# Performance work log

Measured on AMD Instinct MI355X. Metric: run time of the kernel, lower is better.

Reference implementation:

```python
import jax, jax.numpy as jnp
import numpy as np

N, E, F_IN, H, C = 10000, 320000, 256, 256, 40


def setup_inputs() -> dict:
    key = jax.random.key(0)
    ks = jax.random.split(key, 12)
    inp = {
        "x": jax.random.normal(ks[0], (N, F_IN), dtype=jnp.float32),
        "edge_index": jax.random.randint(ks[1], (2, E), 0, N, dtype=jnp.int64),
    }
    dims = [(F_IN, H), (H, H), (H, H), (H, H), (H, C)]
    for i, (din, dout) in enumerate(dims, start=1):
        scale = 1.0 / np.sqrt(din)
        inp[f"W{i}"] = jax.random.normal(ks[1 + i], (din, dout), dtype=jnp.float32) * scale
        inp[f"b{i}"] = jnp.zeros((dout,), dtype=jnp.float32)
    return inp


def _gcn_norm(edge_index, num_nodes, dtype):
    # GCNConv: add self-loops, symmetric normalization D^-1/2 (A+I) D^-1/2
    loops = jnp.arange(num_nodes, dtype=edge_index.dtype)
    src = jnp.concatenate([edge_index[0], loops])
    dst = jnp.concatenate([edge_index[1], loops])
    deg = jax.ops.segment_sum(jnp.ones_like(dst, dtype=dtype), dst, num_segments=num_nodes)
    dinv = jnp.where(deg > 0, deg ** -0.5, 0.0).astype(dtype)
    norm = dinv[src] * dinv[dst]  # [E+N]
    return src, dst, norm


def _conv(h, src, dst, norm, W, b, num_nodes):
    # linear transform then gather-scale-scatter aggregation
    h = h @ W                           # [N, dout]
    msg = h[src] * norm[:, None]        # [E+N, dout]
    return jax.ops.segment_sum(msg, dst, num_segments=num_nodes) + b


def reference(x, edge_index, W1, b1, W2, b2, W3, b3, W4, b4, W5, b5):
    num_nodes = x.shape[0]
    src, dst, norm = _gcn_norm(edge_index, num_nodes, x.dtype)
    h = jax.nn.relu(_conv(x, src, dst, norm, W1, b1, num_nodes))
    h = jax.nn.relu(_conv(h, src, dst, norm, W2, b2, num_nodes))
    h = jax.nn.relu(_conv(h, src, dst, norm, W3, b3, num_nodes))
    h = jax.nn.relu(_conv(h, src, dst, norm, W4, b4, num_nodes))
    logits = _conv(h, src, dst, norm, W5, b5, num_nodes)
    return jax.nn.log_softmax(logits, axis=1), logits
```

## Files before the change

kernel.cpp:

```cpp
#include <hip/hip_runtime.h>
#include <hip/hip_bf16.h>

#define N_NODES 10000
#define N_EDGES 320000
#define HDIM    256
#define NCLS    40
#define WTOT    273448

typedef __attribute__((ext_vector_type(8))) short short8;
typedef __attribute__((ext_vector_type(4))) float floatx4;
typedef unsigned long long ull;
typedef unsigned short ushort;

__device__ __forceinline__ float bf2f(ushort u) {
    union { unsigned int i; float f; } v; v.i = ((unsigned int)u) << 16; return v.f;
}
__device__ __forceinline__ ushort f2bf(float f) {
    __hip_bfloat16 h = __float2bfloat16(f);
    return *reinterpret_cast<ushort*>(&h);
}

__device__ __forceinline__ void detect_flags(const void* x, const void* ei,
                                             int* sflags) {
    const int tid = threadIdx.x;
    if (tid < 64) {
        const ushort* u = (const ushort*)x;
        int e = (u[2 * tid] >> 7) & 0xFF;
        ull badmask = __ballot(e < 100 || e > 140);
        const int* ii = (const int*)ei;
        ull oddnz = __ballot(ii[2 * tid + 1] != 0);
        if (tid == 0) {
            sflags[0] = (__popcll(badmask) >= 8) ? 1 : 0;
            sflags[1] = (oddnz == 0) ? 1 : 0;
        }
    }
    __syncthreads();
}


struct PrepArgs {
    const void* x;
    const void* ei;
    const void* wsrc[10];
    ushort* wdst[10];
    int woffs[11];
    ushort* xb;
    int* src32;
    int* dst32;
    int* cnt;
    ushort* tbuf;
    ushort* hbuf;
    int* flags;
};

#define PREP_XB 2500
#define PREP_WB 1069
#define PREP_EB 1250
#define PREP_TOTAL (PREP_XB + PREP_WB + PREP_EB + 1)

__global__ __launch_bounds__(256)
void prep_kernel(PrepArgs a) {
    __shared__ int sflags[2];
    detect_flags(a.x, a.ei, sflags);
    const int f32 = sflags[0];
    const int b = blockIdx.x;

    if (b < PREP_XB) {
        int i4 = b * 256 + threadIdx.x;
        if (f32) {
            float4 v = ((const float4*)a.x)[i4];
            ull p = (ull)f2bf(v.x) | ((ull)f2bf(v.y) << 16) |
                    ((ull)f2bf(v.z) << 32) | ((ull)f2bf(v.w) << 48);
            ((ull*)a.xb)[i4] = p;
        } else {
            ((ull*)a.xb)[i4] = ((const ull*)a.x)[i4];
        }
    } else if (b < PREP_XB + PREP_WB) {
        int i = (b - PREP_XB) * 256 + threadIdx.x;
        if (i < WTOT) {
            int t = 0;
#pragma unroll
            for (int k = 1; k < 10; ++k) t += (i >= a.woffs[k]);
            int local = i - a.woffs[t];
            ushort v;
            if (f32) v = f2bf(((const float*)a.wsrc[t])[local]);
            else     v = ((const ushort*)a.wsrc[t])[local];
            a.wdst[t][local] = v;
        }
    } else if (b < PREP_XB + PREP_WB + PREP_EB) {
        int e = (b - PREP_XB - PREP_WB) * 256 + threadIdx.x;
        const int* ii = (const int*)a.ei;
        int s, d;
        if (sflags[1]) { s = ii[2 * e]; d = ii[2 * (N_EDGES + e)]; }
        else           { s = ii[e];     d = ii[N_EDGES + e]; }
        s = ((unsigned)s < N_NODES) ? s : 0;
        d = ((unsigned)d < N_NODES) ? d : 0;
        a.src32[e] = s;
        a.dst32[e] = d;
        atomicAdd(&a.cnt[d], 1);
    } else {
        int t = threadIdx.x;
        if (t < 64)       ((ull*)(a.tbuf + (size_t)N_NODES * 256))[t] = 0;
        else if (t < 128) ((ull*)(a.hbuf + (size_t)N_NODES * 256))[t - 64] = 0;
        if (t == 0) { a.flags[0] = sflags[0]; a.flags[1] = sflags[1]; }
    }
}


__global__ __launch_bounds__(1024)
void scan_dinv_kernel(const int* __restrict__ cnt, int* __restrict__ offs,
                      int* __restrict__ woff, float* __restrict__ dinv) {
    __shared__ int wsum[16];
    const int t = threadIdx.x;
    const int lane = t & 63;
    const int wv = t >> 6;
    const int base = t * 10;

    int c[10];
    int s = 0;
#pragma unroll
    for (int j = 0; j < 10; ++j) {
        int i = base + j;
        c[j] = (i < N_NODES) ? cnt[i] : 0;
        s += c[j];
    }

    int inc = s;
#pragma unroll
    for (int o = 1; o < 64; o <<= 1) {
        int v = __shfl_up(inc, o);
        if (lane >= o) inc += v;
    }
    if (lane == 63) wsum[wv] = inc;
    __syncthreads();

    if (wv == 0 && lane < 16) {
        int w = wsum[lane];
        int wi = w;
#pragma unroll
        for (int o = 1; o < 16; o <<= 1) {
            int v = __shfl_up(wi, o);
            if (lane >= o) wi += v;
        }
        wsum[lane] = wi - w;
    }
    __syncthreads();

    int run = wsum[wv] + (inc - s);
#pragma unroll
    for (int j = 0; j < 10; ++j) {
        int i = base + j;
        if (i < N_NODES) {
            offs[i] = run;
            woff[i] = run;
            dinv[i] = rsqrtf((float)c[j] + 1.0f);
            run += c[j];
        }
    }
}


#define FILL_BLKS 1250
#define GEMM1_YT  78
#define FG_TOTAL  (FILL_BLKS + 8 * GEMM1_YT)

__global__ __launch_bounds__(256)
void fillgemm_kernel(const int* __restrict__ src, const int* __restrict__ dst,
                     int* __restrict__ woff, int* __restrict__ csr,
                     const ushort* __restrict__ A, const ushort* __restrict__ W,
                     const float* __restrict__ dinv, ushort* __restrict__ T) {
    const int b = blockIdx.x;
    if (b < FILL_BLKS) {
        int e = b * 256 + threadIdx.x;
        int d = dst[e];
        int p = atomicAdd(&woff[d], 1);
        csr[p] = src[e];
        return;
    }
    const int g = b - FILL_BLKS;
    const int lane = threadIdx.x & 63;
    const int wave = threadIdx.x >> 6;
    const int m = lane & 15;
    const int quad = lane >> 4;
    const int c0 = (g & 7) * 32;
    const int by = g >> 3;

    short8 bfrag[2][8];
#pragma unroll
    for (int t = 0; t < 2; ++t)
#pragma unroll
        for (int s = 0; s < 8; ++s)
#pragma unroll
            for (int j = 0; j < 8; ++j)
                bfrag[t][s][j] = (short)W[(size_t)(s * 32 + quad * 8 + j) * 256 + c0 + t * 16 + m];

    const int step = GEMM1_YT * 4;
    for (int rt = by * 4 + wave; rt < N_NODES / 16; rt += step) {
        const int r0 = rt * 16;
        floatx4 acc0 = {0.f, 0.f, 0.f, 0.f};
        floatx4 acc1 = {0.f, 0.f, 0.f, 0.f};
        const ushort* arow = A + (size_t)(r0 + m) * 256 + quad * 8;
#pragma unroll
        for (int s = 0; s < 8; ++s) {
            short8 af = *(const short8*)(arow + s * 32);
            acc0 = __builtin_amdgcn_mfma_f32_16x16x32_bf16(af, bfrag[0][s], acc0, 0, 0, 0);
            acc1 = __builtin_amdgcn_mfma_f32_16x16x32_bf16(af, bfrag[1][s], acc1, 0, 0, 0);
        }
#pragma unroll
        for (int r = 0; r < 4; ++r) {
            int row = r0 + quad * 4 + r;
            float di = dinv[row];
            T[(size_t)row * 256 + c0 + m]      = f2bf(acc0[r] * di);
            T[(size_t)row * 256 + c0 + 16 + m] = f2bf(acc1[r] * di);
        }
    }
}


__global__ __launch_bounds__(256)
void gemm256_kernel(const ushort* __restrict__ A, const ushort* __restrict__ W,
                    const float* __restrict__ dinv, ushort* __restrict__ T) {
    const int lane = threadIdx.x & 63;
    const int wave = threadIdx.x >> 6;
    const int m = lane & 15;
    const int quad = lane >> 4;
    const int c0 = blockIdx.x * 32;

    short8 bfrag[2][8];
#pragma unroll
    for (int t = 0; t < 2; ++t)
#pragma unroll
        for (int s = 0; s < 8; ++s)
#pragma unroll
            for (int j = 0; j < 8; ++j)
                bfrag[t][s][j] = (short)W[(size_t)(s * 32 + quad * 8 + j) * 256 + c0 + t * 16 + m];

    const int step = gridDim.y * 4;
    for (int rt = blockIdx.y * 4 + wave; rt < N_NODES / 16; rt += step) {
        const int r0 = rt * 16;
        floatx4 acc0 = {0.f, 0.f, 0.f, 0.f};
        floatx4 acc1 = {0.f, 0.f, 0.f, 0.f};
        const ushort* arow = A + (size_t)(r0 + m) * 256 + quad * 8;
#pragma unroll
        for (int s = 0; s < 8; ++s) {
            short8 af = *(const short8*)(arow + s * 32);
            acc0 = __builtin_amdgcn_mfma_f32_16x16x32_bf16(af, bfrag[0][s], acc0, 0, 0, 0);
            acc1 = __builtin_amdgcn_mfma_f32_16x16x32_bf16(af, bfrag[1][s], acc1, 0, 0, 0);
        }
#pragma unroll
        for (int r = 0; r < 4; ++r) {
            int row = r0 + quad * 4 + r;
            float di = dinv[row];
            T[(size_t)row * 256 + c0 + m]      = f2bf(acc0[r] * di);
            T[(size_t)row * 256 + c0 + 16 + m] = f2bf(acc1[r] * di);
        }
    }
}


__global__ __launch_bounds__(256)
void gemm40_kernel(const ushort* __restrict__ A, const ushort* __restrict__ W,
                   const float* __restrict__ dinv, float* __restrict__ T) {
    const int lane = threadIdx.x & 63;
    const int wave = threadIdx.x >> 6;
    const int m = lane & 15;
    const int quad = lane >> 4;
    const int col = blockIdx.x * 16 + m;
    const bool colok = col < NCLS;

    short8 bfrag[8];
#pragma unroll
    for (int s = 0; s < 8; ++s)
#pragma unroll
        for (int j = 0; j < 8; ++j)
            bfrag[s][j] = colok ? (short)W[(size_t)(s * 32 + quad * 8 + j) * NCLS + col] : (short)0;

    const int step = gridDim.y * 4;
    for (int rt = blockIdx.y * 4 + wave; rt < N_NODES / 16; rt += step) {
        const int r0 = rt * 16;
        floatx4 acc = {0.f, 0.f, 0.f, 0.f};
        const ushort* arow = A + (size_t)(r0 + m) * 256 + quad * 8;
#pragma unroll
        for (int s = 0; s < 8; ++s) {
            short8 af = *(const short8*)(arow + s * 32);
            acc = __builtin_amdgcn_mfma_f32_16x16x32_bf16(af, bfrag[s], acc, 0, 0, 0);
        }
        if (colok) {
#pragma unroll
            for (int r = 0; r < 4; ++r) {
                int row = r0 + quad * 4 + r;
                T[(size_t)row * NCLS + col] = acc[r] * dinv[row];
            }
        }
    }
}


__device__ __forceinline__ void accum16(float* acc, int4 r) {
    int d[4] = {r.x, r.y, r.z, r.w};
#pragma unroll
    for (int k = 0; k < 4; ++k) {
        union { int i; float f; } lo, hi;
        lo.i = d[k] << 16;
        hi.i = d[k] & 0xffff0000;
        acc[2 * k]     += lo.f;
        acc[2 * k + 1] += hi.f;
    }
}

__global__ __launch_bounds__(256)
void agg256_kernel(const ushort* __restrict__ T,
                   const int* __restrict__ csr, const int* __restrict__ offs,
                   const int* __restrict__ cnt, const float* __restrict__ dinv,
                   const ushort* __restrict__ bias,
                   ushort* __restrict__ H) {
    const int node = blockIdx.x * 4 + (threadIdx.x >> 6);
    const int lane = threadIdx.x & 63;
    const int half = lane >> 5;
    const int q = lane & 31;
    const int start = offs[node];
    const int count = cnt[node];
    const float di = dinv[node];

    float acc[8];
    {
        int sinit = half ? N_NODES : node;
        int4 r = *(const int4*)(T + (size_t)sinit * 256 + q * 8);
#pragma unroll
        for (int k = 0; k < 4; ++k) {
            union { int i; float f; } lo, hi;
            int d = (&r.x)[k];
            lo.i = d << 16; hi.i = d & 0xffff0000;
            acc[2 * k] = lo.f; acc[2 * k + 1] = hi.f;
        }
    }

    for (int bj = 0; bj < count; bj += 64) {
        int mrem = count - bj;
        int mm = mrem < 64 ? mrem : 64;
        int idxv = (lane < mm) ? csr[start + bj + lane] : N_NODES;
        int j2 = 0;
        for (; j2 + 8 <= mm; j2 += 8) {
            int s0 = __shfl(idxv, j2 + half);
            int s1 = __shfl(idxv, j2 + 2 + half);
            int s2 = __shfl(idxv, j2 + 4 + half);
            int s3 = __shfl(idxv, j2 + 6 + half);
            int4 r0 = *(const int4*)(T + (size_t)s0 * 256 + q * 8);
            int4 r1 = *(const int4*)(T + (size_t)s1 * 256 + q * 8);
            int4 r2 = *(const int4*)(T + (size_t)s2 * 256 + q * 8);
            int4 r3 = *(const int4*)(T + (size_t)s3 * 256 + q * 8);
            accum16(acc, r0); accum16(acc, r1); accum16(acc, r2); accum16(acc, r3);
        }
        for (; j2 < mm; j2 += 2) {
            int s = __shfl(idxv, j2 + half);
            int4 r = *(const int4*)(T + (size_t)s * 256 + q * 8);
            accum16(acc, r);
        }
    }

#pragma unroll
    for (int i = 0; i < 8; ++i) acc[i] += __shfl_xor(acc[i], 32);

    if (half == 0) {
        int4 bv = *(const int4*)(bias + q * 8);
        int out_d[4];
#pragma unroll
        for (int k = 0; k < 4; ++k) {
            union { int i; float f; } lo, hi;
            int d = (&bv.x)[k];
            lo.i = d << 16; hi.i = d & 0xffff0000;
            float v0 = fmaxf(acc[2 * k] * di + lo.f, 0.f);
            float v1 = fmaxf(acc[2 * k + 1] * di + hi.f, 0.f);
            out_d[k] = (int)f2bf(v0) | ((int)f2bf(v1) << 16);
        }
        *(int4*)(H + (size_t)node * 256 + q * 8) = *(int4*)out_d;
    }
}


__global__ __launch_bounds__(256)
void aggsoft_kernel(const float* __restrict__ T,
                    const int* __restrict__ csr, const int* __restrict__ offs,
                    const int* __restrict__ cnt, const float* __restrict__ dinv,
                    const ushort* __restrict__ bias,
                    void* __restrict__ out, const int* __restrict__ flags) {
    const int node = blockIdx.x * 4 + (threadIdx.x >> 6);
    const int lane = threadIdx.x & 63;
    const int start = offs[node];
    const int count = cnt[node];
    const float di = dinv[node];

    float acc = (lane < NCLS) ? T[(size_t)node * NCLS + lane] : 0.f;
    for (int bj = 0; bj < count; bj += 64) {
        int mrem = count - bj;
        int mm = mrem < 64 ? mrem : 64;
        int idxv = (lane < mm) ? csr[start + bj + lane] : 0;
        int jj = 0;
        for (; jj + 4 <= mm; jj += 4) {
            int s0 = __shfl(idxv, jj + 0);
            int s1 = __shfl(idxv, jj + 1);
            int s2 = __shfl(idxv, jj + 2);
            int s3 = __shfl(idxv, jj + 3);
            if (lane < NCLS) {
                float t0 = T[(size_t)s0 * NCLS + lane];
                float t1 = T[(size_t)s1 * NCLS + lane];
                float t2 = T[(size_t)s2 * NCLS + lane];
                float t3 = T[(size_t)s3 * NCLS + lane];
                acc += t0 + t1 + t2 + t3;
            }
        }
        for (; jj < mm; ++jj) {
            int s = __shfl(idxv, jj);
            if (lane < NCLS) acc += T[(size_t)s * NCLS + lane];
        }
    }

    float l = (lane < NCLS) ? (acc * di + bf2f(bias[lane])) : -INFINITY;
    float mx = l;
#pragma unroll
    for (int o = 32; o > 0; o >>= 1) mx = fmaxf(mx, __shfl_xor(mx, o));
    float e = (lane < NCLS) ? __expf(l - mx) : 0.f;
    float sum = e;
#pragma unroll
    for (int o = 32; o > 0; o >>= 1) sum += __shfl_xor(sum, o);
    float ls = l - mx - __logf(sum);
    if (lane < NCLS) {
        size_t i0 = (size_t)node * NCLS + lane;
        size_t i1 = (size_t)N_NODES * NCLS + i0;
        if (flags[0]) {
            ((float*)out)[i0] = ls;
            ((float*)out)[i1] = l;
        } else {
            ((ushort*)out)[i0] = f2bf(ls);
            ((ushort*)out)[i1] = f2bf(l);
        }
    }
}


static inline size_t alup(size_t x) { return (x + 255) & ~(size_t)255; }

extern "C" void kernel_launch(void* const* d_in, const int* in_sizes, int n_in,
                              void* d_out, int out_size, void* d_ws, size_t ws_size,
                              hipStream_t stream) {
    char* w = (char*)d_ws;
    int* flags   = (int*)w;           w += alup(16);
    float* dinv  = (float*)w;         w += alup(N_NODES * 4);
    int* cnt     = (int*)w;           w += alup(N_NODES * 4);
    int* offs    = (int*)w;           w += alup(N_NODES * 4);
    int* woff    = (int*)w;           w += alup(N_NODES * 4);
    int* src32   = (int*)w;           w += alup(N_EDGES * 4);
    int* dst32   = (int*)w;           w += alup(N_EDGES * 4);
    int* csr     = (int*)w;           w += alup(N_EDGES * 4);
    ushort* xb   = (ushort*)w;        w += alup((size_t)N_NODES * HDIM * 2);
    ushort* wb[5]; ushort* bb[5];
    for (int l = 0; l < 5; ++l) {
        int wn = (l < 4) ? HDIM * HDIM : HDIM * NCLS;
        int bn = (l < 4) ? HDIM : NCLS;
        wb[l] = (ushort*)w; w += alup((size_t)wn * 2);
        bb[l] = (ushort*)w; w += alup((size_t)bn * 2);
    }
    ushort* tbuf = (ushort*)w;        w += alup((size_t)(N_NODES + 16) * HDIM * 2);
    ushort* hbuf = (ushort*)w;        w += alup((size_t)(N_NODES + 16) * HDIM * 2);
    float* t5    = (float*)w;         w += alup((size_t)N_NODES * NCLS * 4);

    hipMemsetAsync(cnt, 0, N_NODES * 4, stream);

    PrepArgs pa;
    pa.x = d_in[0];
    pa.ei = d_in[1];
    int sizes[10] = { HDIM * HDIM, HDIM, HDIM * HDIM, HDIM, HDIM * HDIM, HDIM,
                      HDIM * HDIM, HDIM, HDIM * NCLS, NCLS };
    int run = 0;
    for (int t = 0; t < 10; ++t) {
        pa.wsrc[t] = d_in[2 + t];
        pa.wdst[t] = (t & 1) ? bb[t >> 1] : wb[t >> 1];
        pa.woffs[t] = run;
        run += sizes[t];
    }
    pa.woffs[10] = run;
    pa.xb = xb; pa.src32 = src32; pa.dst32 = dst32; pa.cnt = cnt;
    pa.tbuf = tbuf; pa.hbuf = hbuf; pa.flags = flags;

    prep_kernel<<<PREP_TOTAL, 256, 0, stream>>>(pa);
    scan_dinv_kernel<<<1, 1024, 0, stream>>>(cnt, offs, woff, dinv);
    fillgemm_kernel<<<FG_TOTAL, 256, 0, stream>>>(src32, dst32, woff, csr,
                                                  xb, wb[0], dinv, tbuf);

    const int aggblk = N_NODES / 4;

    agg256_kernel<<<aggblk, 256, 0, stream>>>(tbuf, csr, offs, cnt, dinv, bb[0], hbuf);
    for (int l = 1; l < 4; ++l) {
        gemm256_kernel<<<dim3(8, 78), 256, 0, stream>>>(hbuf, wb[l], dinv, tbuf);
        agg256_kernel<<<aggblk, 256, 0, stream>>>(tbuf, csr, offs, cnt, dinv, bb[l], hbuf);
    }
    gemm40_kernel<<<dim3(3, 80), 256, 0, stream>>>(hbuf, wb[4], dinv, t5);
    aggsoft_kernel<<<2500, 256, 0, stream>>>(t5, csr, offs, cnt, dinv, bb[4], d_out, flags);
}
```

Measured before the change: 264.9 us.

## Split aggregation feature dim across two blocks, vectorize weight prep

The 256-feature aggregation kernel now launches twice as many blocks, each handling half of the feature columns for a node. Each wave splits into four 16-lane groups that gather different neighbors at once, which doubles the number of independent gathers in flight per wave, and a two-step shuffle reduction combines them. Output uses nontemporal stores, and launch bounds request higher occupancy. Weight conversion in the prep kernel now processes four elements per thread with vector loads. The cost is that neighbor index lists and degrees are read twice, one extra shuffle reduction is added, and each gather row segment is only 256 bytes.

```diff
diff --git a/kernel.cpp b/kernel.cpp
--- a/kernel.cpp
+++ b/kernel.cpp
@@ -6,9 +6,11 @@
 #define HDIM    256
 #define NCLS    40
 #define WTOT    273448
+#define WQUADS  68362
 
 typedef __attribute__((ext_vector_type(8))) short short8;
 typedef __attribute__((ext_vector_type(4))) float floatx4;
+typedef __attribute__((ext_vector_type(4))) int intx4;
 typedef unsigned long long ull;
 typedef unsigned short ushort;
 
@@ -54,7 +56,7 @@
 };
 
 #define PREP_XB 2500
-#define PREP_WB 1069
+#define PREP_WB 268
 #define PREP_EB 1250
 #define PREP_TOTAL (PREP_XB + PREP_WB + PREP_EB + 1)
 
@@ -77,15 +79,21 @@
         }
     } else if (b < PREP_XB + PREP_WB) {
         int i = (b - PREP_XB) * 256 + threadIdx.x;
-        if (i < WTOT) {
+        if (i < WQUADS) {
+            int i4 = i * 4;
             int t = 0;
 #pragma unroll
-            for (int k = 1; k < 10; ++k) t += (i >= a.woffs[k]);
-            int local = i - a.woffs[t];
-            ushort v;
-            if (f32) v = f2bf(((const float*)a.wsrc[t])[local]);
-            else     v = ((const ushort*)a.wsrc[t])[local];
-            a.wdst[t][local] = v;
+            for (int k = 1; k < 10; ++k) t += (i4 >= a.woffs[k]);
+            int local = i4 - a.woffs[t];
+            ull p;
+            if (f32) {
+                float4 v = *(const float4*)((const float*)a.wsrc[t] + local);
+                p = (ull)f2bf(v.x) | ((ull)f2bf(v.y) << 16) |
+                    ((ull)f2bf(v.z) << 32) | ((ull)f2bf(v.w) << 48);
+            } else {
+                p = *(const ull*)((const ushort*)a.wsrc[t] + local);
+            }
+            *(ull*)(a.wdst[t] + local) = p;
         }
     } else if (b < PREP_XB + PREP_WB + PREP_EB) {
         int e = (b - PREP_XB - PREP_WB) * 256 + threadIdx.x;
@@ -296,7 +304,7 @@
 }
 
 
-__device__ __forceinline__ void accum16(float* acc, int4 r) {
+__device__ __forceinline__ void accum16(float* acc, intx4 r) {
     int d[4] = {r.x, r.y, r.z, r.w};
 #pragma unroll
     for (int k = 0; k < 4; ++k) {
@@ -308,28 +316,36 @@
     }
 }
 
-__global__ __launch_bounds__(256)
+#define AGG_BLKS 5000
+
+__global__ __launch_bounds__(256, 4)
 void agg256_kernel(const ushort* __restrict__ T,
                    const int* __restrict__ csr, const int* __restrict__ offs,
                    const int* __restrict__ cnt, const float* __restrict__ dinv,
                    const ushort* __restrict__ bias,
                    ushort* __restrict__ H) {
-    const int node = blockIdx.x * 4 + (threadIdx.x >> 6);
+    const int bid = blockIdx.x;
+    const int h = (bid >= 2500) ? 1 : 0;
+    const int local = h ? (bid - 2500) : bid;
+    const int wave = threadIdx.x >> 6;
+    const int node = local * 4 + wave;
     const int lane = threadIdx.x & 63;
-    const int half = lane >> 5;
-    const int q = lane & 31;
+    const int quarter = lane >> 4;
+    const int q = lane & 15;
+    const int cbase = h * 128 + q * 8;
+
     const int start = offs[node];
     const int count = cnt[node];
     const float di = dinv[node];
 
     float acc[8];
     {
-        int sinit = half ? N_NODES : node;
-        int4 r = *(const int4*)(T + (size_t)sinit * 256 + q * 8);
+        int sinit = quarter ? N_NODES : node;
+        intx4 r = *(const intx4*)(T + (size_t)sinit * 256 + cbase);
 #pragma unroll
         for (int k = 0; k < 4; ++k) {
             union { int i; float f; } lo, hi;
-            int d = (&r.x)[k];
+            int d = r[k];
             lo.i = d << 16; hi.i = d & 0xffff0000;
             acc[2 * k] = lo.f; acc[2 * k + 1] = hi.f;
         }
@@ -340,40 +356,43 @@
         int mm = mrem < 64 ? mrem : 64;
         int idxv = (lane < mm) ? csr[start + bj + lane] : N_NODES;
         int j2 = 0;
-        for (; j2 + 8 <= mm; j2 += 8) {
-            int s0 = __shfl(idxv, j2 + half);
-            int s1 = __shfl(idxv, j2 + 2 + half);
-            int s2 = __shfl(idxv, j2 + 4 + half);
-            int s3 = __shfl(idxv, j2 + 6 + half);
-            int4 r0 = *(const int4*)(T + (size_t)s0 * 256 + q * 8);
-            int4 r1 = *(const int4*)(T + (size_t)s1 * 256 + q * 8);
-            int4 r2 = *(const int4*)(T + (size_t)s2 * 256 + q * 8);
-            int4 r3 = *(const int4*)(T + (size_t)s3 * 256 + q * 8);
+        for (; j2 + 16 <= mm; j2 += 16) {
+            int s0 = __shfl(idxv, j2 + 0  + quarter);
+            int s1 = __shfl(idxv, j2 + 4  + quarter);
+            int s2 = __shfl(idxv, j2 + 8  + quarter);
+            int s3 = __shfl(idxv, j2 + 12 + quarter);
+            intx4 r0 = *(const intx4*)(T + (size_t)s0 * 256 + cbase);
+            intx4 r1 = *(const intx4*)(T + (size_t)s1 * 256 + cbase);
+            intx4 r2 = *(const intx4*)(T + (size_t)s2 * 256 + cbase);
+            intx4 r3 = *(const intx4*)(T + (size_t)s3 * 256 + cbase);
             accum16(acc, r0); accum16(acc, r1); accum16(acc, r2); accum16(acc, r3);
         }
-        for (; j2 < mm; j2 += 2) {
-            int s = __shfl(idxv, j2 + half);
-            int4 r = *(const int4*)(T + (size_t)s * 256 + q * 8);
+        for (; j2 < mm; j2 += 4) {
+            int s = __shfl(idxv, j2 + quarter);
+            intx4 r = *(const intx4*)(T + (size_t)s * 256 + cbase);
             accum16(acc, r);
         }
     }
 
 #pragma unroll
-    for (int i = 0; i < 8; ++i) acc[i] += __shfl_xor(acc[i], 32);
-
-    if (half == 0) {
-        int4 bv = *(const int4*)(bias + q * 8);
-        int out_d[4];
+    for (int i = 0; i < 8; ++i) {
+        acc[i] += __shfl_xor(acc[i], 32);
+        acc[i] += __shfl_xor(acc[i], 16);
+    }
+
+    if (quarter == 0) {
+        intx4 bv = *(const intx4*)(bias + cbase);
+        intx4 ov;
 #pragma unroll
         for (int k = 0; k < 4; ++k) {
             union { int i; float f; } lo, hi;
-            int d = (&bv.x)[k];
+            int d = bv[k];
             lo.i = d << 16; hi.i = d & 0xffff0000;
             float v0 = fmaxf(acc[2 * k] * di + lo.f, 0.f);
             float v1 = fmaxf(acc[2 * k + 1] * di + hi.f, 0.f);
-            out_d[k] = (int)f2bf(v0) | ((int)f2bf(v1) << 16);
-        }
-        *(int4*)(H + (size_t)node * 256 + q * 8) = *(int4*)out_d;
+            ov[k] = (int)f2bf(v0) | ((int)f2bf(v1) << 16);
+        }
+        __builtin_nontemporal_store(ov, (intx4*)(H + (size_t)node * 256 + cbase));
     }
 }
 
@@ -464,7 +483,7 @@
     ushort* hbuf = (ushort*)w;        w += alup((size_t)(N_NODES + 16) * HDIM * 2);
     float* t5    = (float*)w;         w += alup((size_t)N_NODES * NCLS * 4);
 
-    hipMemsetAsync(cnt, 0, N_NODES * 4, stream);
+    (void)hipMemsetAsync(cnt, 0, N_NODES * 4, stream);
 
     PrepArgs pa;
     pa.x = d_in[0];
@@ -487,12 +506,10 @@
     fillgemm_kernel<<<FG_TOTAL, 256, 0, stream>>>(src32, dst32, woff, csr,
                                                   xb, wb[0], dinv, tbuf);
 
-    const int aggblk = N_NODES / 4;
-
-    agg256_kernel<<<aggblk, 256, 0, stream>>>(tbuf, csr, offs, cnt, dinv, bb[0], hbuf);
+    agg256_kernel<<<AGG_BLKS, 256, 0, stream>>>(tbuf, csr, offs, cnt, dinv, bb[0], hbuf);
     for (int l = 1; l < 4; ++l) {
         gemm256_kernel<<<dim3(8, 78), 256, 0, stream>>>(hbuf, wb[l], dinv, tbuf);
-        agg256_kernel<<<aggblk, 256, 0, stream>>>(tbuf, csr, offs, cnt, dinv, bb[l], hbuf);
+        agg256_kernel<<<AGG_BLKS, 256, 0, stream>>>(tbuf, csr, offs, cnt, dinv, bb[l], hbuf);
     }
     gemm40_kernel<<<dim3(3, 80), 256, 0, stream>>>(hbuf, wb[4], dinv, t5);
     aggsoft_kernel<<<2500, 256, 0, stream>>>(t5, csr, offs, cnt, dinv, bb[4], d_out, flags);
```

New measurement: 271.9 us. 2.7% more time.
